# Kernel optimization log

Hardware: AMD Instinct MI355X
Metric: run time of the kernel (lower is better)

The kernel has to match this reference:

```python
import jax, jax.numpy as jnp
import numpy as np

B, T, F = 1024, 512, 128
HL = 64   # hidden_low
HH = 64   # hidden_high
HIGH_PERIOD = 10
HEAD_HID = 64


def _gru_cell(x, h, Wih, Whh, bih, bhh):
    # PyTorch GRU cell math. x:(B,In) h:(B,H) Wih:(3H,In) Whh:(3H,H)
    gi = x @ Wih.T + bih            # (B,3H)
    gh = h @ Whh.T + bhh            # (B,3H)
    H = h.shape[-1]
    ir, iz, inn = gi[:, :H], gi[:, H:2*H], gi[:, 2*H:]
    hr, hz, hn = gh[:, :H], gh[:, H:2*H], gh[:, 2*H:]
    r = jax.nn.sigmoid(ir + hr)
    z = jax.nn.sigmoid(iz + hz)
    n = jnp.tanh(inn + r * hn)
    return (1.0 - z) * n + z * h


def setup_inputs() -> dict:
    key = jax.random.key(0)
    ks = jax.random.split(key, 14)
    s = 0.05
    return {
        "x": jax.random.normal(ks[0], (B, T, F), dtype=jnp.float32),
        "high_Wih": jax.random.normal(ks[1], (3 * HH, F), dtype=jnp.float32) * s,
        "high_Whh": jax.random.normal(ks[2], (3 * HH, HH), dtype=jnp.float32) * s,
        "high_bih": jax.random.normal(ks[3], (3 * HH,), dtype=jnp.float32) * s,
        "high_bhh": jax.random.normal(ks[4], (3 * HH,), dtype=jnp.float32) * s,
        "low_Wih": jax.random.normal(ks[5], (3 * HL, F + HH), dtype=jnp.float32) * s,
        "low_Whh": jax.random.normal(ks[6], (3 * HL, HL), dtype=jnp.float32) * s,
        "low_bih": jax.random.normal(ks[7], (3 * HL,), dtype=jnp.float32) * s,
        "low_bhh": jax.random.normal(ks[8], (3 * HL,), dtype=jnp.float32) * s,
        "head_W1": jax.random.normal(ks[9], (HEAD_HID, HL), dtype=jnp.float32) * s,
        "head_b1": jax.random.normal(ks[10], (HEAD_HID,), dtype=jnp.float32) * s,
        "head_W2": jax.random.normal(ks[11], (1, HEAD_HID), dtype=jnp.float32) * s,
        "head_b2": jax.random.normal(ks[12], (1,), dtype=jnp.float32) * s,
    }


def reference(x, high_Wih, high_Whh, high_bih, high_bhh,
              low_Wih, low_Whh, low_bih, low_bhh,
              head_W1, head_b1, head_W2, head_b2):
    Bc = x.shape[0]
    # static per-step mask: high GRU updates when t % high_period == 0
    upd_mask = (jnp.arange(T) % HIGH_PERIOD == 0).astype(x.dtype)  # (T,)
    xs = (jnp.swapaxes(x, 0, 1), upd_mask)  # ((T,B,F), (T,))

    def step(carry, inp):
        h_high, h_low = carry
        x_t, m = inp
        h_high_new = _gru_cell(x_t, h_high, high_Wih, high_Whh, high_bih, high_bhh)
        h_high = m * h_high_new + (1.0 - m) * h_high
        low_in = jnp.concatenate([x_t, h_high], axis=-1)  # (B, F+HH)
        h_low = _gru_cell(low_in, h_low, low_Wih, low_Whh, low_bih, low_bhh)
        return (h_high, h_low), None

    h0 = (jnp.zeros((Bc, HH), x.dtype), jnp.zeros((Bc, HL), x.dtype))
    (h_high, h_low), _ = jax.lax.scan(step, h0, xs)

    # head_updown: Linear(HL,64) -> ReLU -> Linear(64,1) -> Sigmoid -> squeeze
    hdn = jax.nn.relu(h_low @ head_W1.T + head_b1)
    p_up = jax.nn.sigmoid(hdn @ head_W2.T + head_b2)[:, 0]  # (B,)
    return p_up
```

## Files before the change

### kernel.cpp

```cpp
#include <hip/hip_runtime.h>
#include <hip/hip_bf16.h>


#define T_STEPS 512
#define F_IN 128

typedef __attribute__((ext_vector_type(8))) short s16x8;
typedef __attribute__((ext_vector_type(4))) float f32x4;

__device__ __forceinline__ float sigm(float v) { return 1.0f / (1.0f + __expf(-v)); }
__device__ __forceinline__ float tanh_fast(float v) { return 1.0f - 2.0f / (__expf(2.0f * v) + 1.0f); }
__device__ __forceinline__ short f2b(float f) {
    __hip_bfloat16 h = __float2bfloat16(f);
    union { __hip_bfloat16 h; short s; } u; u.h = h; return u.s;
}

__global__ void prep_pack(const float* __restrict__ hWih, const float* __restrict__ hWhh,
                          const float* __restrict__ lWih, const float* __restrict__ lWhh,
                          const float* __restrict__ headW1,
                          short* __restrict__ wsS) {
    int i = blockIdx.x * blockDim.x + threadIdx.x;
    if (i < 36864) {
        int j = i & 7, l = (i >> 3) & 63, tile = i >> 9;
        int kt = tile % 6, nt = tile / 6;
        int n = nt * 16 + (l & 15), k = kt * 32 + (l >> 4) * 8 + j;
        wsS[i] = f2b(lWih[n * 192 + k]);
    } else if (i < 49152) {
        int fi = i - 36864;
        int j = fi & 7, l = (fi >> 3) & 63, tile = fi >> 9;
        int kt = tile & 1, nt = tile >> 1;
        int n = nt * 16 + (l & 15), k = kt * 32 + (l >> 4) * 8 + j;
        wsS[i] = f2b(lWhh[n * 64 + k]);
    } else if (i < 73728) {
        int fi = i - 49152;
        int j = fi & 7, l = (fi >> 3) & 63, tile = fi >> 9;
        int kt = tile & 3, nt = tile >> 2;
        int n = nt * 16 + (l & 15), k = kt * 32 + (l >> 4) * 8 + j;
        wsS[i] = f2b(hWih[n * 128 + k]);
    } else if (i < 86016) {
        int fi = i - 73728;
        int j = fi & 7, l = (fi >> 3) & 63, tile = fi >> 9;
        int kt = tile & 1, nt = tile >> 1;
        int n = nt * 16 + (l & 15), k = kt * 32 + (l >> 4) * 8 + j;
        wsS[i] = f2b(hWhh[n * 64 + k]);
    } else if (i < 86016 + 4096) {
        int fi = i - 86016;
        int jj = fi & 63, k = fi >> 6;
        float* W1t = (float*)(wsS + 86016);
        W1t[k * 64 + jj] = headW1[jj * 64 + k];
    }
}

__global__ __launch_bounds__(256, 1)
void hrm_mfma(const float* __restrict__ x,
              const float* __restrict__ high_bih, const float* __restrict__ high_bhh,
              const float* __restrict__ low_bih,  const float* __restrict__ low_bhh,
              const float* __restrict__ head_b1,  const float* __restrict__ head_W2,
              const float* __restrict__ head_b2,
              const short* __restrict__ wsS,
              float* __restrict__ out) {
    const int tid = threadIdx.x;
    const int w = tid >> 6, l = tid & 63;
    const int lo4 = l & 15, hi4 = l >> 4;
    const int j = w * 16 + lo4;

    const s16x8* pLGi = (const s16x8*)wsS;
    const s16x8* pLGh = (const s16x8*)(wsS + 36864);
    const s16x8* pHGi = (const s16x8*)(wsS + 49152);
    const s16x8* pHGh = (const s16x8*)(wsS + 73728);
    const float* W1t  = (const float*)(wsS + 86016);

    __shared__ __align__(16) short Ahl[2][16 * 72];
    __shared__ __align__(16) short Ahh[16 * 72];
    __shared__ float hlf[16][68];

    for (int i = tid; i < 2 * 16 * 72; i += 256) ((short*)Ahl)[i] = 0;
    for (int i = tid; i < 16 * 72; i += 256) Ahh[i] = 0;

    float lbi[3], lbh[3], hbi[3], hbh[3];
    #pragma unroll
    for (int g = 0; g < 3; ++g) {
        lbi[g] = low_bih[g * 64 + j];  lbh[g] = low_bhh[g * 64 + j];
        hbi[g] = high_bih[g * 64 + j]; hbh[g] = high_bhh[g * 64 + j];
    }

    s16x8 Bgi[3][6], Bgh[3][2];
    #pragma unroll
    for (int g = 0; g < 3; ++g) {
        #pragma unroll
        for (int kt = 0; kt < 6; ++kt) Bgi[g][kt] = pLGi[((g * 4 + w) * 6 + kt) * 64 + l];
        #pragma unroll
        for (int kt = 0; kt < 2; ++kt) Bgh[g][kt] = pLGh[((g * 4 + w) * 2 + kt) * 64 + l];
    }

    float hl[4] = {0.f, 0.f, 0.f, 0.f};
    float hh[4] = {0.f, 0.f, 0.f, 0.f};

    const int r0 = blockIdx.x * 4;
    const float* xlane = x + ((size_t)(r0 + (lo4 & 3)) * T_STEPS) * F_IN + hi4 * 8;

    f32x4 xraw[4][2];
    #pragma unroll
    for (int kt = 0; kt < 4; ++kt) {
        xraw[kt][0] = *(const f32x4*)(xlane + kt * 32);
        xraw[kt][1] = *(const f32x4*)(xlane + kt * 32 + 4);
    }

    __syncthreads();

    int tmod = 0;
    for (int t = 0; t < T_STEPS; ++t) {
        s16x8 xf[4];
        #pragma unroll
        for (int kt = 0; kt < 4; ++kt) {
            union { s16x8 v; __hip_bfloat162 h2[4]; } u;
            u.h2[0] = __float22bfloat162_rn(make_float2(xraw[kt][0].x, xraw[kt][0].y));
            u.h2[1] = __float22bfloat162_rn(make_float2(xraw[kt][0].z, xraw[kt][0].w));
            u.h2[2] = __float22bfloat162_rn(make_float2(xraw[kt][1].x, xraw[kt][1].y));
            u.h2[3] = __float22bfloat162_rn(make_float2(xraw[kt][1].z, xraw[kt][1].w));
            xf[kt] = u.v;
        }

        const int rb = t & 1, wbf = rb ^ 1;

        if (tmod == 0) {
            s16x8 ah0 = *(const s16x8*)&Ahh[lo4 * 72 + hi4 * 8];
            s16x8 ah1 = *(const s16x8*)&Ahh[lo4 * 72 + 32 + hi4 * 8];
            f32x4 gi[3], gh[3];
            #pragma unroll
            for (int g = 0; g < 3; ++g) {
                gi[g] = (f32x4){hbi[g], hbi[g], hbi[g], hbi[g]};
                gh[g] = (f32x4){hbh[g], hbh[g], hbh[g], hbh[g]};
            }
            #pragma unroll
            for (int g = 0; g < 3; ++g) {
                s16x8 b0 = pHGh[((g * 4 + w) * 2 + 0) * 64 + l];
                s16x8 b1 = pHGh[((g * 4 + w) * 2 + 1) * 64 + l];
                gh[g] = __builtin_amdgcn_mfma_f32_16x16x32_bf16(ah0, b0, gh[g], 0, 0, 0);
                gh[g] = __builtin_amdgcn_mfma_f32_16x16x32_bf16(ah1, b1, gh[g], 0, 0, 0);
            }
            #pragma unroll
            for (int g = 0; g < 3; ++g) {
                #pragma unroll
                for (int kt = 0; kt < 4; ++kt) {
                    s16x8 b = pHGi[((g * 4 + w) * 4 + kt) * 64 + l];
                    gi[g] = __builtin_amdgcn_mfma_f32_16x16x32_bf16(xf[kt], b, gi[g], 0, 0, 0);
                }
            }
            #pragma unroll
            for (int q = 0; q < 4; ++q) {
                float r = sigm(gi[0][q] + gh[0][q]);
                float z = sigm(gi[1][q] + gh[1][q]);
                float n = tanh_fast(gi[2][q] + r * gh[2][q]);
                hh[q] = (1.0f - z) * n + z * hh[q];
            }
            __syncthreads();
            #pragma unroll
            for (int q = 0; q < 4; ++q)
                Ahh[(hi4 * 4 + q) * 72 + j] = f2b(hh[q]);
            __syncthreads();
        }
        if (++tmod == 10) tmod = 0;

        s16x8 al0 = *(const s16x8*)&Ahl[rb][lo4 * 72 + hi4 * 8];
        s16x8 al1 = *(const s16x8*)&Ahl[rb][lo4 * 72 + 32 + hi4 * 8];
        s16x8 ah0 = *(const s16x8*)&Ahh[lo4 * 72 + hi4 * 8];
        s16x8 ah1 = *(const s16x8*)&Ahh[lo4 * 72 + 32 + hi4 * 8];

        f32x4 gi[3], gh[3];
        #pragma unroll
        for (int g = 0; g < 3; ++g) {
            gi[g] = (f32x4){lbi[g], lbi[g], lbi[g], lbi[g]};
            gh[g] = (f32x4){lbh[g], lbh[g], lbh[g], lbh[g]};
        }
        #pragma unroll
        for (int g = 0; g < 3; ++g) {
            gh[g] = __builtin_amdgcn_mfma_f32_16x16x32_bf16(al0, Bgh[g][0], gh[g], 0, 0, 0);
            gh[g] = __builtin_amdgcn_mfma_f32_16x16x32_bf16(al1, Bgh[g][1], gh[g], 0, 0, 0);
        }
        #pragma unroll
        for (int g = 0; g < 3; ++g) {
            #pragma unroll
            for (int kt = 0; kt < 4; ++kt)
                gi[g] = __builtin_amdgcn_mfma_f32_16x16x32_bf16(xf[kt], Bgi[g][kt], gi[g], 0, 0, 0);
            gi[g] = __builtin_amdgcn_mfma_f32_16x16x32_bf16(ah0, Bgi[g][4], gi[g], 0, 0, 0);
            gi[g] = __builtin_amdgcn_mfma_f32_16x16x32_bf16(ah1, Bgi[g][5], gi[g], 0, 0, 0);
        }

        if (t + 1 < T_STEPS) {
            #pragma unroll
            for (int kt = 0; kt < 4; ++kt) {
                xraw[kt][0] = *(const f32x4*)(xlane + (size_t)(t + 1) * F_IN + kt * 32);
                xraw[kt][1] = *(const f32x4*)(xlane + (size_t)(t + 1) * F_IN + kt * 32 + 4);
            }
        }

        #pragma unroll
        for (int q = 0; q < 4; ++q) {
            float r = sigm(gi[0][q] + gh[0][q]);
            float z = sigm(gi[1][q] + gh[1][q]);
            float n = tanh_fast(gi[2][q] + r * gh[2][q]);
            hl[q] = (1.0f - z) * n + z * hl[q];
        }
        #pragma unroll
        for (int q = 0; q < 4; ++q)
            Ahl[wbf][(hi4 * 4 + q) * 72 + j] = f2b(hl[q]);
        __syncthreads();
    }

    #pragma unroll
    for (int q = 0; q < 4; ++q) hlf[hi4 * 4 + q][j] = hl[q];
    __syncthreads();

    float hd = head_b1[l];
    for (int k = 0; k < 64; ++k)
        hd = fmaf(hlf[w][k], W1t[k * 64 + l], hd);
    hd = fmaxf(hd, 0.0f);
    float v = hd * head_W2[l];
    #pragma unroll
    for (int off = 32; off > 0; off >>= 1) v += __shfl_down(v, off);
    if (l == 0) out[r0 + w] = sigm(v + head_b2[0]);
}

extern "C" void kernel_launch(void* const* d_in, const int* in_sizes, int n_in,
                              void* d_out, int out_size, void* d_ws, size_t ws_size,
                              hipStream_t stream) {
    (void)in_sizes; (void)n_in; (void)out_size; (void)ws_size;
    const float* x        = (const float*)d_in[0];
    const float* high_Wih = (const float*)d_in[1];
    const float* high_Whh = (const float*)d_in[2];
    const float* high_bih = (const float*)d_in[3];
    const float* high_bhh = (const float*)d_in[4];
    const float* low_Wih  = (const float*)d_in[5];
    const float* low_Whh  = (const float*)d_in[6];
    const float* low_bih  = (const float*)d_in[7];
    const float* low_bhh  = (const float*)d_in[8];
    const float* head_W1  = (const float*)d_in[9];
    const float* head_b1  = (const float*)d_in[10];
    const float* head_W2  = (const float*)d_in[11];
    const float* head_b2  = (const float*)d_in[12];
    short* wsS = (short*)d_ws;
    float* out = (float*)d_out;

    prep_pack<<<352, 256, 0, stream>>>(high_Wih, high_Whh, low_Wih, low_Whh, head_W1, wsS);
    hrm_mfma<<<256, 256, 0, stream>>>(x, high_bih, high_bhh, low_bih, low_bhh,
                                      head_b1, head_W2, head_b2, wsS, out);
}
```

Before: 988.5 us.

## Split batch into 2-row blocks, double-buffer high state, deepen x prefetch

Each block now handles 2 batch rows instead of 4, so 512 blocks launch and two blocks can sit on each CU (launch_bounds 256,2). This spreads the serial recurrence across more CUs and lets waves from different blocks hide each other's latency. The high-GRU hidden buffer is double-buffered, removing one barrier per high update. x loads are prefetched two steps ahead, and the MFMA accumulation is split into two independent chains to shorten dependency latency. The cost is that MFMA row slots are half-wasted (16-row tiles carry only 2 real rows) and register pressure rises under the tighter occupancy bound.

```diff
diff --git a/kernel.cpp b/kernel.cpp
--- a/kernel.cpp
+++ b/kernel.cpp
@@ -51,7 +51,7 @@
     }
 }
 
-__global__ __launch_bounds__(256, 1)
+__global__ __launch_bounds__(256, 2)
 void hrm_mfma(const float* __restrict__ x,
               const float* __restrict__ high_bih, const float* __restrict__ high_bhh,
               const float* __restrict__ low_bih,  const float* __restrict__ low_bhh,
@@ -71,11 +71,11 @@
     const float* W1t  = (const float*)(wsS + 86016);
 
     __shared__ __align__(16) short Ahl[2][16 * 72];
-    __shared__ __align__(16) short Ahh[16 * 72];
+    __shared__ __align__(16) short Ahh[2][16 * 72];
     __shared__ float hlf[16][68];
 
     for (int i = tid; i < 2 * 16 * 72; i += 256) ((short*)Ahl)[i] = 0;
-    for (int i = tid; i < 16 * 72; i += 256) Ahh[i] = 0;
+    for (int i = tid; i < 2 * 16 * 72; i += 256) ((short*)Ahh)[i] = 0;
 
     float lbi[3], lbh[3], hbi[3], hbh[3];
     #pragma unroll
@@ -96,41 +96,52 @@
     float hl[4] = {0.f, 0.f, 0.f, 0.f};
     float hh[4] = {0.f, 0.f, 0.f, 0.f};
 
-    const int r0 = blockIdx.x * 4;
-    const float* xlane = x + ((size_t)(r0 + (lo4 & 3)) * T_STEPS) * F_IN + hi4 * 8;
-
-    f32x4 xraw[4][2];
+    const int r0 = blockIdx.x * 2;
+    const float* xlane = x + ((size_t)(r0 + (lo4 & 1)) * T_STEPS) * F_IN + hi4 * 8;
+
+    f32x4 xraw[2][4][2];
     #pragma unroll
     for (int kt = 0; kt < 4; ++kt) {
-        xraw[kt][0] = *(const f32x4*)(xlane + kt * 32);
-        xraw[kt][1] = *(const f32x4*)(xlane + kt * 32 + 4);
+        xraw[0][kt][0] = *(const f32x4*)(xlane + kt * 32);
+        xraw[0][kt][1] = *(const f32x4*)(xlane + kt * 32 + 4);
+        xraw[1][kt][0] = *(const f32x4*)(xlane + F_IN + kt * 32);
+        xraw[1][kt][1] = *(const f32x4*)(xlane + F_IN + kt * 32 + 4);
     }
 
     __syncthreads();
 
-    int tmod = 0;
+    int tmod = 0, hb = 0;
     for (int t = 0; t < T_STEPS; ++t) {
+        const int cur = t & 1;
         s16x8 xf[4];
         #pragma unroll
         for (int kt = 0; kt < 4; ++kt) {
             union { s16x8 v; __hip_bfloat162 h2[4]; } u;
-            u.h2[0] = __float22bfloat162_rn(make_float2(xraw[kt][0].x, xraw[kt][0].y));
-            u.h2[1] = __float22bfloat162_rn(make_float2(xraw[kt][0].z, xraw[kt][0].w));
-            u.h2[2] = __float22bfloat162_rn(make_float2(xraw[kt][1].x, xraw[kt][1].y));
-            u.h2[3] = __float22bfloat162_rn(make_float2(xraw[kt][1].z, xraw[kt][1].w));
+            u.h2[0] = __float22bfloat162_rn(make_float2(xraw[cur][kt][0].x, xraw[cur][kt][0].y));
+            u.h2[1] = __float22bfloat162_rn(make_float2(xraw[cur][kt][0].z, xraw[cur][kt][0].w));
+            u.h2[2] = __float22bfloat162_rn(make_float2(xraw[cur][kt][1].x, xraw[cur][kt][1].y));
+            u.h2[3] = __float22bfloat162_rn(make_float2(xraw[cur][kt][1].z, xraw[cur][kt][1].w));
             xf[kt] = u.v;
         }
-
-        const int rb = t & 1, wbf = rb ^ 1;
+        if (t + 2 < T_STEPS) {
+            #pragma unroll
+            for (int kt = 0; kt < 4; ++kt) {
+                xraw[cur][kt][0] = *(const f32x4*)(xlane + (size_t)(t + 2) * F_IN + kt * 32);
+                xraw[cur][kt][1] = *(const f32x4*)(xlane + (size_t)(t + 2) * F_IN + kt * 32 + 4);
+            }
+        }
+
+        const int rb = cur, wbf = cur ^ 1;
 
         if (tmod == 0) {
-            s16x8 ah0 = *(const s16x8*)&Ahh[lo4 * 72 + hi4 * 8];
-            s16x8 ah1 = *(const s16x8*)&Ahh[lo4 * 72 + 32 + hi4 * 8];
-            f32x4 gi[3], gh[3];
+            s16x8 ah0 = *(const s16x8*)&Ahh[hb][lo4 * 72 + hi4 * 8];
+            s16x8 ah1 = *(const s16x8*)&Ahh[hb][lo4 * 72 + 32 + hi4 * 8];
+            f32x4 giA[3], giB[3], gh[3];
             #pragma unroll
             for (int g = 0; g < 3; ++g) {
-                gi[g] = (f32x4){hbi[g], hbi[g], hbi[g], hbi[g]};
-                gh[g] = (f32x4){hbh[g], hbh[g], hbh[g], hbh[g]};
+                giA[g] = (f32x4){hbi[g], hbi[g], hbi[g], hbi[g]};
+                giB[g] = (f32x4){0.f, 0.f, 0.f, 0.f};
+                gh[g]  = (f32x4){hbh[g], hbh[g], hbh[g], hbh[g]};
             }
             #pragma unroll
             for (int g = 0; g < 3; ++g) {
@@ -141,37 +152,44 @@
             }
             #pragma unroll
             for (int g = 0; g < 3; ++g) {
-                #pragma unroll
-                for (int kt = 0; kt < 4; ++kt) {
-                    s16x8 b = pHGi[((g * 4 + w) * 4 + kt) * 64 + l];
-                    gi[g] = __builtin_amdgcn_mfma_f32_16x16x32_bf16(xf[kt], b, gi[g], 0, 0, 0);
-                }
+                s16x8 b0 = pHGi[((g * 4 + w) * 4 + 0) * 64 + l];
+                s16x8 b1 = pHGi[((g * 4 + w) * 4 + 1) * 64 + l];
+                s16x8 b2 = pHGi[((g * 4 + w) * 4 + 2) * 64 + l];
+                s16x8 b3 = pHGi[((g * 4 + w) * 4 + 3) * 64 + l];
+                giA[g] = __builtin_amdgcn_mfma_f32_16x16x32_bf16(xf[0], b0, giA[g], 0, 0, 0);
+                giB[g] = __builtin_amdgcn_mfma_f32_16x16x32_bf16(xf[2], b2, giB[g], 0, 0, 0);
+                giA[g] = __builtin_amdgcn_mfma_f32_16x16x32_bf16(xf[1], b1, giA[g], 0, 0, 0);
+                giB[g] = __builtin_amdgcn_mfma_f32_16x16x32_bf16(xf[3], b3, giB[g], 0, 0, 0);
             }
             #pragma unroll
             for (int q = 0; q < 4; ++q) {
-                float r = sigm(gi[0][q] + gh[0][q]);
-                float z = sigm(gi[1][q] + gh[1][q]);
-                float n = tanh_fast(gi[2][q] + r * gh[2][q]);
+                float gi0 = giA[0][q] + giB[0][q];
+                float gi1 = giA[1][q] + giB[1][q];
+                float gi2 = giA[2][q] + giB[2][q];
+                float r = sigm(gi0 + gh[0][q]);
+                float z = sigm(gi1 + gh[1][q]);
+                float n = tanh_fast(gi2 + r * gh[2][q]);
                 hh[q] = (1.0f - z) * n + z * hh[q];
             }
+            #pragma unroll
+            for (int q = 0; q < 4; ++q)
+                Ahh[hb ^ 1][(hi4 * 4 + q) * 72 + j] = f2b(hh[q]);
             __syncthreads();
-            #pragma unroll
-            for (int q = 0; q < 4; ++q)
-                Ahh[(hi4 * 4 + q) * 72 + j] = f2b(hh[q]);
-            __syncthreads();
+            hb ^= 1;
         }
         if (++tmod == 10) tmod = 0;
 
         s16x8 al0 = *(const s16x8*)&Ahl[rb][lo4 * 72 + hi4 * 8];
         s16x8 al1 = *(const s16x8*)&Ahl[rb][lo4 * 72 + 32 + hi4 * 8];
-        s16x8 ah0 = *(const s16x8*)&Ahh[lo4 * 72 + hi4 * 8];
-        s16x8 ah1 = *(const s16x8*)&Ahh[lo4 * 72 + 32 + hi4 * 8];
-
-        f32x4 gi[3], gh[3];
+        s16x8 ah0 = *(const s16x8*)&Ahh[hb][lo4 * 72 + hi4 * 8];
+        s16x8 ah1 = *(const s16x8*)&Ahh[hb][lo4 * 72 + 32 + hi4 * 8];
+
+        f32x4 giA[3], giB[3], gh[3];
         #pragma unroll
         for (int g = 0; g < 3; ++g) {
-            gi[g] = (f32x4){lbi[g], lbi[g], lbi[g], lbi[g]};
-            gh[g] = (f32x4){lbh[g], lbh[g], lbh[g], lbh[g]};
+            giA[g] = (f32x4){lbi[g], lbi[g], lbi[g], lbi[g]};
+            giB[g] = (f32x4){0.f, 0.f, 0.f, 0.f};
+            gh[g]  = (f32x4){lbh[g], lbh[g], lbh[g], lbh[g]};
         }
         #pragma unroll
         for (int g = 0; g < 3; ++g) {
@@ -180,26 +198,22 @@
         }
         #pragma unroll
         for (int g = 0; g < 3; ++g) {
-            #pragma unroll
-            for (int kt = 0; kt < 4; ++kt)
-                gi[g] = __builtin_amdgcn_mfma_f32_16x16x32_bf16(xf[kt], Bgi[g][kt], gi[g], 0, 0, 0);
-            gi[g] = __builtin_amdgcn_mfma_f32_16x16x32_bf16(ah0, Bgi[g][4], gi[g], 0, 0, 0);
-            gi[g] = __builtin_amdgcn_mfma_f32_16x16x32_bf16(ah1, Bgi[g][5], gi[g], 0, 0, 0);
-        }
-
-        if (t + 1 < T_STEPS) {
-            #pragma unroll
-            for (int kt = 0; kt < 4; ++kt) {
-                xraw[kt][0] = *(const f32x4*)(xlane + (size_t)(t + 1) * F_IN + kt * 32);
-                xraw[kt][1] = *(const f32x4*)(xlane + (size_t)(t + 1) * F_IN + kt * 32 + 4);
-            }
+            giA[g] = __builtin_amdgcn_mfma_f32_16x16x32_bf16(xf[0], Bgi[g][0], giA[g], 0, 0, 0);
+            giB[g] = __builtin_amdgcn_mfma_f32_16x16x32_bf16(xf[2], Bgi[g][2], giB[g], 0, 0, 0);
+            giA[g] = __builtin_amdgcn_mfma_f32_16x16x32_bf16(xf[1], Bgi[g][1], giA[g], 0, 0, 0);
+            giB[g] = __builtin_amdgcn_mfma_f32_16x16x32_bf16(xf[3], Bgi[g][3], giB[g], 0, 0, 0);
+            giA[g] = __builtin_amdgcn_mfma_f32_16x16x32_bf16(ah0, Bgi[g][4], giA[g], 0, 0, 0);
+            giB[g] = __builtin_amdgcn_mfma_f32_16x16x32_bf16(ah1, Bgi[g][5], giB[g], 0, 0, 0);
         }
 
         #pragma unroll
         for (int q = 0; q < 4; ++q) {
-            float r = sigm(gi[0][q] + gh[0][q]);
-            float z = sigm(gi[1][q] + gh[1][q]);
-            float n = tanh_fast(gi[2][q] + r * gh[2][q]);
+            float gi0 = giA[0][q] + giB[0][q];
+            float gi1 = giA[1][q] + giB[1][q];
+            float gi2 = giA[2][q] + giB[2][q];
+            float r = sigm(gi0 + gh[0][q]);
+            float z = sigm(gi1 + gh[1][q]);
+            float n = tanh_fast(gi2 + r * gh[2][q]);
             hl[q] = (1.0f - z) * n + z * hl[q];
         }
         #pragma unroll
@@ -212,14 +226,16 @@
     for (int q = 0; q < 4; ++q) hlf[hi4 * 4 + q][j] = hl[q];
     __syncthreads();
 
-    float hd = head_b1[l];
-    for (int k = 0; k < 64; ++k)
-        hd = fmaf(hlf[w][k], W1t[k * 64 + l], hd);
-    hd = fmaxf(hd, 0.0f);
-    float v = hd * head_W2[l];
-    #pragma unroll
-    for (int off = 32; off > 0; off >>= 1) v += __shfl_down(v, off);
-    if (l == 0) out[r0 + w] = sigm(v + head_b2[0]);
+    if (w < 2) {
+        float hd = head_b1[l];
+        for (int k = 0; k < 64; ++k)
+            hd = fmaf(hlf[w][k], W1t[k * 64 + l], hd);
+        hd = fmaxf(hd, 0.0f);
+        float v = hd * head_W2[l];
+        #pragma unroll
+        for (int off = 32; off > 0; off >>= 1) v += __shfl_down(v, off);
+        if (l == 0) out[r0 + w] = sigm(v + head_b2[0]);
+    }
 }
 
 extern "C" void kernel_launch(void* const* d_in, const int* in_sizes, int n_in,
@@ -243,6 +259,6 @@
     float* out = (float*)d_out;
 
     prep_pack<<<352, 256, 0, stream>>>(high_Wih, high_Whh, low_Wih, low_Whh, head_W1, wsS);
-    hrm_mfma<<<256, 256, 0, stream>>>(x, high_bih, high_bhh, low_bih, low_bhh,
+    hrm_mfma<<<512, 256, 0, stream>>>(x, high_bih, high_bhh, low_bih, low_bhh,
                                       head_b1, head_W2, head_b2, wsS, out);
 }
```

Result: slower. 3.686 ms (+272.9%).
